# Performance work log

Hardware: AMD Instinct MI355X
Metric: run time of the kernel (lower is better)

Reference implementation:

```python
import jax, jax.numpy as jnp
import numpy as np

N = 10000      # nodes
E = 160000     # edges (before self loops)
F_IN = 78      # atom features
C = 128        # output_dim per head
H = 10         # heads in gat1
G = 64         # graphs in batch


def gat_conv(x, src, dst, n_nodes, W, a_src, a_dst, heads, ch):
    # x: [N, Fin]; W: [Fin, heads*ch]; a_src/a_dst: [heads, ch]
    h = (x @ W).reshape(-1, heads, ch)                      # [N, H, C]
    alpha_src = (h * a_src).sum(-1)                         # [N, H]
    alpha_dst = (h * a_dst).sum(-1)                         # [N, H]
    e = jax.nn.leaky_relu(alpha_src[src] + alpha_dst[dst], 0.2)  # [E, H]
    # segment softmax over edges grouped by destination node
    m = jax.ops.segment_max(e, dst, num_segments=n_nodes)
    m = jnp.where(jnp.isfinite(m), m, 0.0)
    ex = jnp.exp(e - m[dst])
    den = jax.ops.segment_sum(ex, dst, num_segments=n_nodes)
    alpha = ex / (den[dst] + 1e-16)                         # [E, H]
    out = jax.ops.segment_sum(h[src] * alpha[:, :, None], dst,
                              num_segments=n_nodes)          # [N, H, C]
    return out, alpha


def setup_inputs() -> dict:
    key = jax.random.key(0)
    ks = jax.random.split(key, 12)
    x = jax.random.normal(ks[0], (N, F_IN), dtype=jnp.float32)
    edge_index = jax.random.randint(ks[1], (2, E), 0, N, dtype=jnp.int64)
    batch = jnp.sort(jax.random.randint(ks[2], (N,), 0, G, dtype=jnp.int64))
    s1 = 1.0 / np.sqrt(F_IN)
    s2 = 1.0 / np.sqrt(H * C)
    W1 = jax.random.normal(ks[3], (F_IN, H * C), jnp.float32) * s1
    att_src1 = jax.random.normal(ks[4], (H, C), jnp.float32) * 0.1
    att_dst1 = jax.random.normal(ks[5], (H, C), jnp.float32) * 0.1
    b1 = jnp.zeros((H * C,), jnp.float32)
    W2 = jax.random.normal(ks[6], (H * C, C), jnp.float32) * s2
    att_src2 = jax.random.normal(ks[7], (1, C), jnp.float32) * 0.1
    att_dst2 = jax.random.normal(ks[8], (1, C), jnp.float32) * 0.1
    b2 = jnp.zeros((C,), jnp.float32)
    return {"x": x, "edge_index": edge_index, "batch": batch,
            "W1": W1, "att_src1": att_src1, "att_dst1": att_dst1, "b1": b1,
            "W2": W2, "att_src2": att_src2, "att_dst2": att_dst2, "b2": b2}


def reference(x, edge_index, batch, W1, att_src1, att_dst1, b1,
              W2, att_src2, att_dst2, b2):
    n = x.shape[0]
    loops = jnp.arange(n, dtype=edge_index.dtype)
    src = jnp.concatenate([edge_index[0], loops])  # PyG adds self loops
    dst = jnp.concatenate([edge_index[1], loops])
    # layer 1: 10 heads, concat
    h1, alpha1 = gat_conv(x, src, dst, n, W1, att_src1, att_dst1, H, C)
    h1 = jax.nn.elu(h1.reshape(n, H * C) + b1)     # dropout skipped (eval)
    # layer 2: 1 head
    h2, _ = gat_conv(h1, src, dst, n, W2, att_src2, att_dst2, 1, C)
    h2 = jax.nn.elu(h2.reshape(n, C) + b2)
    # global max pool per graph
    pooled = jax.ops.segment_max(h2, batch, num_segments=G)  # [G, C]
    return pooled, alpha1
```

## Files before the change

### kernel.cpp

```cpp
#include <hip/hip_runtime.h>
#include <hip/hip_bf16.h>

#define FIN 78
#define CDIM 128
#define HEADS 10
#define HC 1280
#define GRAPHS 64
#define KP 96

typedef __bf16 bf16x8 __attribute__((ext_vector_type(8)));
typedef __bf16 bf16x4 __attribute__((ext_vector_type(4)));
typedef float f32x4 __attribute__((ext_vector_type(4)));

__global__ void init_kernel(unsigned* counts, unsigned* cursor, unsigned* pooled_u,
                            float* as1, float* ad1,
                            const float* __restrict__ x, __bf16* __restrict__ xb,
                            const float* __restrict__ W1, __bf16* __restrict__ W1t,
                            const float* __restrict__ W2, __bf16* __restrict__ W2t,
                            int N, int Mpad) {
    int t = blockIdx.x * 256 + threadIdx.x;
    if (t < N) { counts[t] = 0u; cursor[t] = 0u; }
    if (t < GRAPHS * CDIM) pooled_u[t] = 0x007FFFFFu;
    if (t < N * HEADS) { as1[t] = 0.f; ad1[t] = 0.f; }
    if (t < Mpad * KP) {
        int m = t / KP, k = t % KP;
        float v = (m < N && k < FIN) ? x[(size_t)m * FIN + k] : 0.f;
        xb[t] = (__bf16)v;
    }
    if (t < HC * KP) {
        int n = t / KP, k = t % KP;
        float v = (k < FIN) ? W1[(size_t)k * HC + n] : 0.f;
        W1t[t] = (__bf16)v;
    }
    if (t < CDIM * HC) {
        int n = t / HC, k = t % HC;
        W2t[t] = (__bf16)W2[(size_t)k * CDIM + n];
    }
}

__global__ void hist_kernel(const int* __restrict__ ei, int E, unsigned* counts) {
    int e = blockIdx.x * 256 + threadIdx.x;
    if (e < E) atomicAdd(&counts[ei[E + e]], 1u);
}

__global__ __launch_bounds__(256) void gemm1_mfma_kernel(
        const __bf16* __restrict__ xb, const __bf16* __restrict__ W1t,
        const float* __restrict__ asrc, const float* __restrict__ adst,
        __bf16* __restrict__ h1pb, float* __restrict__ as1, float* __restrict__ ad1,
        int M) {
    __shared__ __align__(16) __bf16 smem[2 * 128 * 104];
    auto Alds = (__bf16 (*)[104])smem;
    auto Blds = (__bf16 (*)[104])(smem + 128 * 104);
    const int tid = threadIdx.x;
    const int wave = tid >> 6, lane = tid & 63;
    const int wr = wave >> 1, wc = wave & 1;
    const int m0 = blockIdx.x * 128;
    const int head = blockIdx.y;
    const int n0 = head * CDIM;
    const int fl = lane & 15;
    const int fh = lane >> 4;

    for (int idx = tid; idx < 128 * 12; idx += 256) {
        int r = idx / 12, ks = (idx % 12) * 8;
        *(bf16x8*)&Alds[r][ks] = *(const bf16x8*)(xb + (size_t)(m0 + r) * KP + ks);
        *(bf16x8*)&Blds[r][ks] = *(const bf16x8*)(W1t + (size_t)(n0 + r) * KP + ks);
    }
    __syncthreads();

    f32x4 acc[4][4] = {};
    #pragma unroll
    for (int ks = 0; ks < KP; ks += 32) {
        bf16x8 a[4], b[4];
        #pragma unroll
        for (int t = 0; t < 4; ++t) {
            a[t] = *(const bf16x8*)&Alds[wr * 64 + t * 16 + fl][ks + fh * 8];
            b[t] = *(const bf16x8*)&Blds[wc * 64 + t * 16 + fl][ks + fh * 8];
        }
        #pragma unroll
        for (int i = 0; i < 4; ++i)
            #pragma unroll
            for (int j = 0; j < 4; ++j)
                acc[i][j] = __builtin_amdgcn_mfma_f32_16x16x32_bf16(a[i], b[j], acc[i][j], 0, 0, 0);
    }

    float a_s[4], a_d[4];
    #pragma unroll
    for (int j = 0; j < 4; ++j) {
        int gn = n0 + wc * 64 + j * 16 + fl;
        a_s[j] = asrc[gn];
        a_d[j] = adst[gn];
    }
    #pragma unroll
    for (int i = 0; i < 4; ++i) {
        #pragma unroll
        for (int r = 0; r < 4; ++r) {
            int gm = m0 + wr * 64 + i * 16 + fh * 4 + r;
            float vs = 0.f, vd = 0.f;
            #pragma unroll
            for (int j = 0; j < 4; ++j) {
                vs += acc[i][j][r] * a_s[j];
                vd += acc[i][j][r] * a_d[j];
            }
            #pragma unroll
            for (int off = 1; off < 16; off <<= 1) {
                vs += __shfl_xor(vs, off);
                vd += __shfl_xor(vd, off);
            }
            if (fl == 0 && gm < M) {
                atomicAdd(&as1[gm * HEADS + head], vs);
                atomicAdd(&ad1[gm * HEADS + head], vd);
            }
        }
    }

    __syncthreads();
    auto Cst = (__bf16 (*)[136])smem;
    #pragma unroll
    for (int i = 0; i < 4; ++i)
        #pragma unroll
        for (int j = 0; j < 4; ++j)
            #pragma unroll
            for (int r = 0; r < 4; ++r)
                Cst[wr * 64 + i * 16 + fh * 4 + r][wc * 64 + j * 16 + fl] = (__bf16)acc[i][j][r];
    __syncthreads();
    for (int idx = tid; idx < 128 * 16; idx += 256) {
        int r = idx >> 4, v = (idx & 15) * 8;
        int gm = m0 + r;
        if (gm < M)
            *(bf16x8*)(h1pb + (size_t)gm * HC + n0 + v) = *(const bf16x8*)&Cst[r][v];
    }
}

__global__ __launch_bounds__(256) void gemm2_mfma_kernel(
        const __bf16* __restrict__ A, const __bf16* __restrict__ W2t,
        float* __restrict__ Cpart, int M) {
    constexpr int BK = 64;
    constexpr int KCHUNK = HC / 2;
    __shared__ __align__(16) __bf16 smem[2 * 64 * 72];
    auto Alds = (__bf16 (*)[72])smem;
    auto Blds = (__bf16 (*)[72])(smem + 64 * 72);
    const int tid = threadIdx.x;
    const int wave = tid >> 6, lane = tid & 63;
    const int wr = wave >> 1, wc = wave & 1;
    const int m0 = blockIdx.x * 64;
    const int n0 = blockIdx.y * 64;
    const int kbase = blockIdx.z * KCHUNK;

    const int kslot = (tid & 7) * 8;
    const int srow  = tid >> 3;
    const int fl = lane & 15;
    const int fh = lane >> 4;

    f32x4 acc[2][2] = {};

    for (int k0 = kbase; k0 < kbase + KCHUNK; k0 += BK) {
        #pragma unroll
        for (int rp = 0; rp < 2; ++rp) {
            int r = srow + rp * 32;
            int gm = m0 + r;
            bf16x8 va = {};
            if (gm < M) va = *(const bf16x8*)(A + (size_t)gm * HC + k0 + kslot);
            *(bf16x8*)&Alds[r][kslot] = va;
            *(bf16x8*)&Blds[r][kslot] = *(const bf16x8*)(W2t + (size_t)(n0 + r) * HC + k0 + kslot);
        }
        __syncthreads();
        #pragma unroll
        for (int ks = 0; ks < BK; ks += 32) {
            bf16x8 a[2], b[2];
            #pragma unroll
            for (int t = 0; t < 2; ++t) {
                a[t] = *(const bf16x8*)&Alds[wr * 32 + t * 16 + fl][ks + fh * 8];
                b[t] = *(const bf16x8*)&Blds[wc * 32 + t * 16 + fl][ks + fh * 8];
            }
            #pragma unroll
            for (int i = 0; i < 2; ++i)
                #pragma unroll
                for (int j = 0; j < 2; ++j)
                    acc[i][j] = __builtin_amdgcn_mfma_f32_16x16x32_bf16(a[i], b[j], acc[i][j], 0, 0, 0);
        }
        __syncthreads();
    }
    auto CstF = (float (*)[68])smem;
    #pragma unroll
    for (int i = 0; i < 2; ++i)
        #pragma unroll
        for (int j = 0; j < 2; ++j)
            #pragma unroll
            for (int r = 0; r < 4; ++r)
                CstF[wr * 32 + i * 16 + fh * 4 + r][wc * 32 + j * 16 + fl] = acc[i][j][r];
    __syncthreads();
    float* base = Cpart + (size_t)blockIdx.z * M * CDIM;
    for (int idx = tid; idx < 64 * 16; idx += 256) {
        int r = idx >> 4, c = (idx & 15) * 4;
        int gm = m0 + r;
        if (gm < M)
            *(f32x4*)(base + (size_t)gm * CDIM + n0 + c) = *(const f32x4*)&CstF[r][c];
    }
}

__global__ __launch_bounds__(256) void combine_kernel(
        const float* __restrict__ Cpart, const float* __restrict__ asrc2,
        const float* __restrict__ adst2, __bf16* __restrict__ h2b,
        float* __restrict__ as2, float* __restrict__ ad2, int N) {
    const int lane = threadIdx.x & 63, wave = threadIdx.x >> 6;
    const int n = blockIdx.x * 4 + wave;
    if (n >= N) return;
    const float* p0 = Cpart + (size_t)n * CDIM;
    const float* p1 = Cpart + (size_t)(N + n) * CDIM;
    float v0 = p0[lane] + p1[lane];
    float v1 = p0[lane + 64] + p1[lane + 64];
    h2b[(size_t)n * CDIM + lane] = (__bf16)v0;
    h2b[(size_t)n * CDIM + lane + 64] = (__bf16)v1;
    float vs = v0 * asrc2[lane] + v1 * asrc2[lane + 64];
    float vd = v0 * adst2[lane] + v1 * adst2[lane + 64];
    #pragma unroll
    for (int off = 32; off; off >>= 1) {
        vs += __shfl_xor(vs, off);
        vd += __shfl_xor(vd, off);
    }
    if (lane == 0) { as2[n] = vs; ad2[n] = vd; }
}

__global__ void scan_kernel(const unsigned* __restrict__ counts, unsigned* __restrict__ offsets, int n) {
    __shared__ unsigned part[1024];
    int t = threadIdx.x;
    int chunk = (n + 1023) / 1024;
    int lo = t * chunk, hi = min(lo + chunk, n);
    unsigned s = 0;
    for (int i = lo; i < hi; ++i) s += counts[i] + 1u;
    part[t] = s;
    __syncthreads();
    for (int d = 1; d < 1024; d <<= 1) {
        unsigned v = (t >= d) ? part[t - d] : 0u;
        __syncthreads();
        part[t] += v;
        __syncthreads();
    }
    unsigned base = (t == 0) ? 0u : part[t - 1];
    for (int i = lo; i < hi; ++i) { offsets[i] = base; base += counts[i] + 1u; }
    if (t == 1023) offsets[n] = part[1023];
}

__global__ void scatter_kernel(const int* __restrict__ ei, int E, int N,
                               const unsigned* __restrict__ offsets, unsigned* cursor,
                               int2* __restrict__ csr2) {
    int e = blockIdx.x * 256 + threadIdx.x;
    int Et = E + N;
    if (e >= Et) return;
    int s, d;
    if (e < E) { s = ei[e]; d = ei[E + e]; } else { s = e - E; d = e - E; }
    unsigned pos = offsets[d] + atomicAdd(&cursor[d], 1u);
    csr2[pos] = make_int2(s, e);
}

__global__ __launch_bounds__(256) void softmax1_kernel(
        const unsigned* __restrict__ offsets, const int2* __restrict__ csr2,
        const float* __restrict__ as1, const float* __restrict__ ad1,
        float* __restrict__ alpha_out, float* __restrict__ alpha_csr, int N) {
    const int wave = threadIdx.x >> 6, lane = threadIdx.x & 63;
    const int n = blockIdx.x * 4 + wave;
    if (n >= N) return;
    const unsigned p0 = offsets[n], p1 = offsets[n + 1];
    const unsigned deg = p1 - p0;

    float adn[HEADS];
    #pragma unroll
    for (int h = 0; h < HEADS; ++h) adn[h] = ad1[n * HEADS + h];

    if (deg <= 64) {
        const bool act = lane < (int)deg;
        const unsigned p = p0 + lane;
        int s = 0, eid = 0;
        if (act) { int2 se = csr2[p]; s = se.x; eid = se.y; }
        const float* arow = as1 + (size_t)s * HEADS;
        float e[HEADS];
        #pragma unroll
        for (int h = 0; h < HEADS; ++h) {
            float v = act ? (arow[h] + adn[h]) : -INFINITY;
            e[h] = (v >= 0.f) ? v : 0.2f * v;
        }
        float m[HEADS];
        #pragma unroll
        for (int h = 0; h < HEADS; ++h) m[h] = e[h];
        #pragma unroll
        for (int off = 32; off; off >>= 1)
            #pragma unroll
            for (int h = 0; h < HEADS; ++h) m[h] = fmaxf(m[h], __shfl_xor(m[h], off));
        float ex[HEADS], sm[HEADS];
        #pragma unroll
        for (int h = 0; h < HEADS; ++h) {
            ex[h] = act ? __expf(e[h] - m[h]) : 0.f;
            sm[h] = ex[h];
        }
        #pragma unroll
        for (int off = 32; off; off >>= 1)
            #pragma unroll
            for (int h = 0; h < HEADS; ++h) sm[h] += __shfl_xor(sm[h], off);
        if (act) {
            #pragma unroll
            for (int h = 0; h < HEADS; ++h) {
                float a = ex[h] / (sm[h] + 1e-16f);
                alpha_csr[(size_t)p * HEADS + h] = a;
                alpha_out[(size_t)eid * HEADS + h] = a;
            }
        }
    } else {
        float m[HEADS];
        #pragma unroll
        for (int h = 0; h < HEADS; ++h) m[h] = -INFINITY;
        for (unsigned p = p0 + lane; p < p1; p += 64) {
            const float* arow = as1 + (size_t)csr2[p].x * HEADS;
            #pragma unroll
            for (int h = 0; h < HEADS; ++h) {
                float v = arow[h] + adn[h];
                v = (v >= 0.f) ? v : 0.2f * v;
                m[h] = fmaxf(m[h], v);
            }
        }
        #pragma unroll
        for (int off = 32; off; off >>= 1)
            #pragma unroll
            for (int h = 0; h < HEADS; ++h) m[h] = fmaxf(m[h], __shfl_xor(m[h], off));
        float sm[HEADS];
        #pragma unroll
        for (int h = 0; h < HEADS; ++h) sm[h] = 0.f;
        for (unsigned p = p0 + lane; p < p1; p += 64) {
            const float* arow = as1 + (size_t)csr2[p].x * HEADS;
            #pragma unroll
            for (int h = 0; h < HEADS; ++h) {
                float v = arow[h] + adn[h];
                v = (v >= 0.f) ? v : 0.2f * v;
                sm[h] += __expf(v - m[h]);
            }
        }
        #pragma unroll
        for (int off = 32; off; off >>= 1)
            #pragma unroll
            for (int h = 0; h < HEADS; ++h) sm[h] += __shfl_xor(sm[h], off);
        float inv[HEADS];
        #pragma unroll
        for (int h = 0; h < HEADS; ++h) inv[h] = 1.f / (sm[h] + 1e-16f);
        for (unsigned p = p0 + lane; p < p1; p += 64) {
            int2 se = csr2[p];
            const float* arow = as1 + (size_t)se.x * HEADS;
            #pragma unroll
            for (int h = 0; h < HEADS; ++h) {
                float v = arow[h] + adn[h];
                v = (v >= 0.f) ? v : 0.2f * v;
                float a = __expf(v - m[h]) * inv[h];
                alpha_csr[(size_t)p * HEADS + h] = a;
                alpha_out[(size_t)se.y * HEADS + h] = a;
            }
        }
    }
}

__global__ __launch_bounds__(160) void agg1_kernel(
        const unsigned* __restrict__ offsets, const int2* __restrict__ csr2,
        const float* __restrict__ alpha_csr, const __bf16* __restrict__ h1pb,
        const float* __restrict__ b1, __bf16* __restrict__ h1b, int N) {
    __shared__ float a_lds[64 * 2];
    __shared__ int s_lds[64];
    const int c = blockIdx.x & 7;
    const int n = blockIdx.x >> 3;
    const int tid = threadIdx.x;
    const int col = c * 160 + tid;
    const int h0 = (c * 160) >> 7;
    const int hl = (col >> 7) - h0;
    const unsigned p0 = offsets[n], p1 = offsets[n + 1];
    float acc = 0.f;
    for (unsigned base = p0; base < p1; base += 64) {
        int cnt = (int)min(64u, p1 - base);
        for (int idx = tid; idx < cnt * 2; idx += 160) {
            int j = idx >> 1, hh = idx & 1;
            a_lds[idx] = alpha_csr[(size_t)(base + j) * HEADS + h0 + hh];
        }
        for (int idx = tid; idx < cnt; idx += 160) s_lds[idx] = csr2[base + idx].x;
        __syncthreads();
        #pragma unroll 4
        for (int j = 0; j < cnt; ++j) {
            float hv = (float)h1pb[(size_t)s_lds[j] * HC + col];
            acc += hv * a_lds[j * 2 + hl];
        }
        __syncthreads();
    }
    float v = acc + b1[col];
    v = (v > 0.f) ? v : expm1f(v);
    h1b[(size_t)n * HC + col] = (__bf16)v;
}

__device__ __forceinline__ unsigned enc_f(float f) {
    unsigned b = __float_as_uint(f);
    return (b & 0x80000000u) ? ~b : (b | 0x80000000u);
}
__device__ __forceinline__ float dec_f(unsigned k) {
    return (k & 0x80000000u) ? __uint_as_float(k & 0x7FFFFFFFu) : __uint_as_float(~k);
}

__global__ __launch_bounds__(128) void agg2_kernel(
        const unsigned* __restrict__ offsets, const int2* __restrict__ csr2,
        const float* __restrict__ as2, const float* __restrict__ ad2,
        const __bf16* __restrict__ h2b, const float* __restrict__ b2,
        const int* __restrict__ batch, unsigned* __restrict__ pooled_u, int N) {
    const int n = blockIdx.x;
    const int tid = threadIdx.x;
    const int lane = tid & 63;
    const unsigned p0 = offsets[n], p1 = offsets[n + 1];
    const int deg = (int)(p1 - p0);
    const float adn = ad2[n];
    float acc = 0.f;

    if (deg <= 64) {
        int s_reg = 0;
        float e_reg = -INFINITY;
        if (lane < deg) {
            s_reg = csr2[p0 + lane].x;
            float v = as2[s_reg] + adn;
            e_reg = (v >= 0.f) ? v : 0.2f * v;
        }
        float m = e_reg;
        #pragma unroll
        for (int off = 32; off; off >>= 1) m = fmaxf(m, __shfl_xor(m, off));
        float ex = (lane < deg) ? __expf(e_reg - m) : 0.f;
        float den = ex;
        #pragma unroll
        for (int off = 32; off; off >>= 1) den += __shfl_xor(den, off);
        float inv = 1.f / (den + 1e-16f);
        for (int j = 0; j < deg; ++j) {
            int sj = __shfl(s_reg, j);
            float aj = __shfl(ex, j) * inv;
            acc += (float)h2b[(size_t)sj * CDIM + tid] * aj;
        }
    } else {
        float m = -INFINITY;
        for (unsigned p = p0 + lane; p < p1; p += 64) {
            float v = as2[csr2[p].x] + adn;
            v = (v >= 0.f) ? v : 0.2f * v;
            m = fmaxf(m, v);
        }
        #pragma unroll
        for (int off = 32; off; off >>= 1) m = fmaxf(m, __shfl_xor(m, off));
        float den = 0.f;
        for (unsigned p = p0 + lane; p < p1; p += 64) {
            float v = as2[csr2[p].x] + adn;
            v = (v >= 0.f) ? v : 0.2f * v;
            den += __expf(v - m);
        }
        #pragma unroll
        for (int off = 32; off; off >>= 1) den += __shfl_xor(den, off);
        float inv = 1.f / (den + 1e-16f);
        for (unsigned p = p0; p < p1; ++p) {
            int sj = csr2[p].x;
            float v = as2[sj] + adn;
            v = (v >= 0.f) ? v : 0.2f * v;
            float aj = __expf(v - m) * inv;
            acc += (float)h2b[(size_t)sj * CDIM + tid] * aj;
        }
    }
    float v = acc + b2[tid];
    v = (v > 0.f) ? v : expm1f(v);
    atomicMax(&pooled_u[batch[n] * CDIM + tid], enc_f(v));
}

__global__ void pool_write_kernel(const unsigned* __restrict__ pooled_u, float* __restrict__ out) {
    int t = blockIdx.x * 256 + threadIdx.x;
    if (t < GRAPHS * CDIM) out[t] = dec_f(pooled_u[t]);
}

extern "C" void kernel_launch(void* const* d_in, const int* in_sizes, int n_in,
                              void* d_out, int out_size, void* d_ws, size_t ws_size,
                              hipStream_t stream) {
    const float* x     = (const float*)d_in[0];
    const int*   ei    = (const int*)d_in[1];
    const int*   batch = (const int*)d_in[2];
    const float* W1    = (const float*)d_in[3];
    const float* asrc1 = (const float*)d_in[4];
    const float* adst1 = (const float*)d_in[5];
    const float* b1    = (const float*)d_in[6];
    const float* W2    = (const float*)d_in[7];
    const float* asrc2 = (const float*)d_in[8];
    const float* adst2 = (const float*)d_in[9];
    const float* b2    = (const float*)d_in[10];
    float* out = (float*)d_out;

    const int N  = in_sizes[0] / FIN;
    const int E  = in_sizes[1] / 2;
    const int Et = E + N;
    const int Mpad = ((N + 127) / 128) * 128;

    char* w = (char*)d_ws;
    auto alloc = [&](size_t nbytes) {
        char* p = w;
        w += (nbytes + 255) & ~(size_t)255;
        return p;
    };
    __bf16* h1pb = (__bf16*)alloc((size_t)N * HC * 2);
    __bf16* h1b  = (__bf16*)alloc((size_t)N * HC * 2);
    __bf16* xb   = (__bf16*)alloc((size_t)Mpad * KP * 2);
    __bf16* W1t  = (__bf16*)alloc((size_t)HC * KP * 2);
    __bf16* W2t  = (__bf16*)alloc((size_t)CDIM * HC * 2);
    float*  Cpart = (float*)alloc((size_t)2 * N * CDIM * 4);
    __bf16* h2b  = (__bf16*)alloc((size_t)N * CDIM * 2);
    float*  as1  = (float*)alloc((size_t)N * HEADS * 4);
    float*  ad1  = (float*)alloc((size_t)N * HEADS * 4);
    float*  as2  = (float*)alloc((size_t)N * 4);
    float*  ad2  = (float*)alloc((size_t)N * 4);
    float*  alpha_csr = (float*)alloc((size_t)Et * HEADS * 4);
    unsigned* counts  = (unsigned*)alloc((size_t)N * 4);
    unsigned* cursor  = (unsigned*)alloc((size_t)N * 4);
    unsigned* offsets = (unsigned*)alloc((size_t)(N + 1) * 4);
    int2* csr2 = (int2*)alloc((size_t)Et * 8);
    unsigned* pooled_u = (unsigned*)alloc((size_t)GRAPHS * CDIM * 4);

    float* alpha_out = out + GRAPHS * CDIM;

    const int init_work = Mpad * KP;
    init_kernel<<<(init_work + 255) / 256, 256, 0, stream>>>(
        counts, cursor, pooled_u, as1, ad1, x, xb, W1, W1t, W2, W2t, N, Mpad);

    gemm1_mfma_kernel<<<dim3(Mpad / 128, HEADS), 256, 0, stream>>>(
        xb, W1t, asrc1, adst1, h1pb, as1, ad1, N);

    hist_kernel<<<(E + 255) / 256, 256, 0, stream>>>(ei, E, counts);
    scan_kernel<<<1, 1024, 0, stream>>>(counts, offsets, N);
    scatter_kernel<<<(Et + 255) / 256, 256, 0, stream>>>(ei, E, N, offsets, cursor, csr2);

    softmax1_kernel<<<(N + 3) / 4, 256, 0, stream>>>(
        offsets, csr2, as1, ad1, alpha_out, alpha_csr, N);
    agg1_kernel<<<N * 8, 160, 0, stream>>>(offsets, csr2, alpha_csr, h1pb, b1, h1b, N);

    gemm2_mfma_kernel<<<dim3((N + 63) / 64, CDIM / 64, 2), 256, 0, stream>>>(
        h1b, W2t, Cpart, N);
    combine_kernel<<<(N + 3) / 4, 256, 0, stream>>>(Cpart, asrc2, adst2, h2b, as2, ad2, N);

    agg2_kernel<<<N, 128, 0, stream>>>(offsets, csr2, as2, ad2, h2b, b2, batch, pooled_u, N);

    pool_write_kernel<<<(GRAPHS * CDIM + 255) / 256, 256, 0, stream>>>(pooled_u, out);
}
```

Measured before the change: 323.0 us.

## Vectorize agg1 gathers to 16-byte loads with edge-parallel slots and LDS reduction

The layer-1 aggregation kernel now splits its 160 threads into 8 edge slots of 20 threads. Each thread loads 8 contiguous bf16 features with one 16-byte load, so the block handles 8 edges at once. The 8 partial sums per column are then reduced through shared memory before bias and ELU. This cuts the number of narrow 2-byte gathers and adds memory-level parallelism, at the cost of extra LDS traffic, a final sync, and 8 accumulators per thread.

```diff
diff --git a/kernel.cpp b/kernel.cpp
--- a/kernel.cpp
+++ b/kernel.cpp
@@ -9,7 +9,6 @@
 #define KP 96
 
 typedef __bf16 bf16x8 __attribute__((ext_vector_type(8)));
-typedef __bf16 bf16x4 __attribute__((ext_vector_type(4)));
 typedef float f32x4 __attribute__((ext_vector_type(4)));
 
 __global__ void init_kernel(unsigned* counts, unsigned* cursor, unsigned* pooled_u,
@@ -361,14 +360,17 @@
         const float* __restrict__ b1, __bf16* __restrict__ h1b, int N) {
     __shared__ float a_lds[64 * 2];
     __shared__ int s_lds[64];
+    __shared__ float red[8][168];
     const int c = blockIdx.x & 7;
     const int n = blockIdx.x >> 3;
     const int tid = threadIdx.x;
-    const int col = c * 160 + tid;
+    const int slot = tid / 20;
+    const int cc = tid % 20;
+    const int col0 = c * 160 + cc * 8;
     const int h0 = (c * 160) >> 7;
-    const int hl = (col >> 7) - h0;
+    const int hl = (col0 >> 7) - h0;
     const unsigned p0 = offsets[n], p1 = offsets[n + 1];
-    float acc = 0.f;
+    float acc[8] = {};
     for (unsigned base = p0; base < p1; base += 64) {
         int cnt = (int)min(64u, p1 - base);
         for (int idx = tid; idx < cnt * 2; idx += 160) {
@@ -377,16 +379,25 @@
         }
         for (int idx = tid; idx < cnt; idx += 160) s_lds[idx] = csr2[base + idx].x;
         __syncthreads();
-        #pragma unroll 4
-        for (int j = 0; j < cnt; ++j) {
-            float hv = (float)h1pb[(size_t)s_lds[j] * HC + col];
-            acc += hv * a_lds[j * 2 + hl];
+        for (int j8 = 0; j8 < cnt; j8 += 8) {
+            int e = j8 + slot;
+            if (e < cnt) {
+                bf16x8 hv = *(const bf16x8*)(h1pb + (size_t)s_lds[e] * HC + col0);
+                float a = a_lds[e * 2 + hl];
+                #pragma unroll
+                for (int k = 0; k < 8; ++k) acc[k] += (float)hv[k] * a;
+            }
         }
         __syncthreads();
     }
-    float v = acc + b1[col];
+    #pragma unroll
+    for (int k = 0; k < 8; ++k) red[slot][cc * 8 + k] = acc[k];
+    __syncthreads();
+    float v = red[0][tid] + red[1][tid] + red[2][tid] + red[3][tid]
+            + red[4][tid] + red[5][tid] + red[6][tid] + red[7][tid];
+    v += b1[c * 160 + tid];
     v = (v > 0.f) ? v : expm1f(v);
-    h1b[(size_t)n * HC + col] = (__bf16)v;
+    h1b[(size_t)n * HC + c * 160 + tid] = (__bf16)v;
 }
 
 __device__ __forceinline__ unsigned enc_f(float f) {
```

New measurement: 299.6 us. 1.08x faster.
